# Kernel tuning notes

Measured on AMD Instinct MI355X. Metric: run time of the kernel, lower is better.

The kernel has to match this reference:

```python
import jax, jax.numpy as jnp
import numpy as np

B, C, LATENT = 64, 64, 256
KS = [50, 25, 12]  # grid side per stage; nodes 2500 -> 625 -> 144 -> 36
EPS = 1e-5


def _grid_graph(k):
    """torch_geometric.utils.grid: 8-neighbor stencil + self-loop, symmetric.
    Returns (src, dst, norm) with GCN symmetric normalization D^-1/2 A D^-1/2."""
    ii, jj = np.meshgrid(np.arange(k), np.arange(k), indexing='ij')
    src_l, dst_l = [], []
    for di in (-1, 0, 1):
        for dj in (-1, 0, 1):
            i0, i1 = max(0, -di), k - max(0, di)
            j0, j1 = max(0, -dj), k - max(0, dj)
            a = (ii[i0:i1, j0:j1] * k + jj[i0:i1, j0:j1]).ravel()
            b = ((ii[i0:i1, j0:j1] + di) * k + (jj[i0:i1, j0:j1] + dj)).ravel()
            src_l.append(a); dst_l.append(b)
    src = np.concatenate(src_l); dst = np.concatenate(dst_l)
    deg = np.bincount(dst, minlength=k * k).astype(np.float32)
    norm = 1.0 / np.sqrt(deg[src] * deg[dst])
    return jnp.asarray(src), jnp.asarray(dst), jnp.asarray(norm.astype(np.float32))

GRAPHS = [_grid_graph(k) for k in KS]


def _gcn(x, W, b, graph):
    # x: [B, N, Cin]; GCNConv: aggregate(norm * (xW)) + b
    src, dst, norm = graph
    h = x @ W                                   # [B, N, Cout]
    msg = h[:, src, :] * norm[None, :, None]    # gather along node dim
    out = jnp.zeros(h.shape, h.dtype).at[:, dst, :].add(msg)
    return out + b


def _inorm(x):
    # torch InstanceNorm1d applied to [B, N, C]: normalize over last axis
    m = jnp.mean(x, axis=-1, keepdims=True)
    v = jnp.var(x, axis=-1, keepdims=True)
    return (x - m) * jax.lax.rsqrt(v + EPS)


def _block(x, k, W1, b1, W2, b2, graph):
    x1 = jax.nn.celu(_inorm(_gcn(x, W1, b1, graph)))
    x2 = jax.nn.celu(_inorm(_gcn(x1, W2, b2, graph)) + x)
    Bn, N, Cc = x2.shape
    g = jnp.swapaxes(x2.reshape(Bn, k, k, Cc), 1, 3)      # [B, C, k, k]
    kk = (k // 2) * 2
    g = g[:, :, :kk, :kk].reshape(Bn, Cc, k // 2, 2, k // 2, 2).max(axis=(3, 5))
    return jnp.swapaxes(g, 1, 3).reshape(Bn, (k // 2) ** 2, Cc)


def _sn_linear(x, W, b, iters=30):
    # spectral-norm Linear: y = x @ (W / sigma_max(W)).T + b (power iteration)
    u = jnp.ones((W.shape[0],), W.dtype) / jnp.sqrt(jnp.asarray(W.shape[0], W.dtype))
    for _ in range(iters):
        v = W.T @ u
        v = v / (jnp.linalg.norm(v) + 1e-12)
        u = W @ v
        u = u / (jnp.linalg.norm(u) + 1e-12)
    sigma = u @ (W @ v)
    return x @ (W / sigma).T + b


def _forward(x, w_init, b_init, w11, b11, w12, b12, w21, b21, w22, b22,
             w31, b31, w32, b32, lw1, lb1, lw2, lb2):
    h = _gcn(x, w_init, b_init, GRAPHS[0])                 # [B, 2500, 64]
    h = _block(h, KS[0], w11, b11, w12, b12, GRAPHS[0])    # [B, 625, 64]
    h = _block(h, KS[1], w21, b21, w22, b22, GRAPHS[1])    # [B, 144, 64]
    h = _block(h, KS[2], w31, b31, w32, b32, GRAPHS[2])    # [B, 36, 64]
    h = h.reshape(h.shape[0], -1)                          # [B, 2304]
    h = jax.nn.celu(_sn_linear(h, lw1, lb1))
    h = jax.nn.celu(_sn_linear(h, lw2, lb2))
    return h


def setup_inputs() -> dict:
    key = jax.random.key(0)
    ks = jax.random.split(key, 20)
    n = lambda k, shape, fan: jax.random.normal(k, shape, jnp.float32) / np.sqrt(fan)
    flat = 36 * C
    return {
        'x': jax.random.normal(ks[0], (B, 2500, 1), jnp.float32),
        'w_init': n(ks[1], (1, C), 1), 'b_init': jnp.zeros((C,), jnp.float32),
        'w11': n(ks[2], (C, C), C), 'b11': jnp.zeros((C,), jnp.float32),
        'w12': n(ks[3], (C, C), C), 'b12': jnp.zeros((C,), jnp.float32),
        'w21': n(ks[4], (C, C), C), 'b21': jnp.zeros((C,), jnp.float32),
        'w22': n(ks[5], (C, C), C), 'b22': jnp.zeros((C,), jnp.float32),
        'w31': n(ks[6], (C, C), C), 'b31': jnp.zeros((C,), jnp.float32),
        'w32': n(ks[7], (C, C), C), 'b32': jnp.zeros((C,), jnp.float32),
        'lw1': n(ks[8], (LATENT, flat), flat), 'lb1': jnp.zeros((LATENT,), jnp.float32),
        'lw2': n(ks[9], (LATENT, LATENT), LATENT), 'lb2': jnp.zeros((LATENT,), jnp.float32),
    }


def reference(x, w_init, b_init, w11, b11, w12, b12, w21, b21, w22, b22,
              w31, b31, w32, b32, lw1, lb1, lw2, lb2):
    return _forward(x, w_init, b_init, w11, b11, w12, b12, w21, b21, w22, b22,
                    w31, b31, w32, b32, lw1, lb1, lw2, lb2)
```

## Files before the change

kernel.cpp:

```cpp
#include <hip/hip_runtime.h>
#include <hip/hip_bf16.h>
#include <math.h>

#define BATCH 64
#define K1 50
#define K2 25
#define K3 12
#define N1 (K1*K1)
#define N2 (K2*K2)
#define N3 (K3*K3)
#define EPS_IN 1e-5f

#define IRT2 0.70710678118654752f
#define IRT3 0.57735026918962576f

typedef __bf16 bf16x4 __attribute__((ext_vector_type(4)));
typedef __bf16 bf16x8 __attribute__((ext_vector_type(8)));
typedef float  f32x4  __attribute__((ext_vector_type(4)));

__device__ __forceinline__ float celu1(float v) {
    return v > 0.f ? v : (__expf(v) - 1.0f);
}

__device__ __forceinline__ float bfac(int v, int K) {
    return (v > 0 && v < K - 1) ? IRT3 : IRT2;
}

__global__ __launch_bounds__(256) void stencil_kernel(
    const float* __restrict__ x, float* __restrict__ out)
{
    int node = blockIdx.x * 256 + threadIdx.x;
    int b = node / N1, n = node - b * N1;
    int i = n / K1, j = n - i * K1;

    float fi[3], fj[3];
    int ric[3], rjc[3];
    {
        int im = i - 1, ip = i + 1;
        ric[0] = im < 0 ? 0 : im;       fi[0] = im < 0 ? 0.f : bfac(im, K1);
        ric[1] = i;                     fi[1] = bfac(i, K1);
        ric[2] = ip >= K1 ? K1-1 : ip;  fi[2] = ip >= K1 ? 0.f : bfac(ip, K1);
        int jm = j - 1, jp = j + 1;
        rjc[0] = jm < 0 ? 0 : jm;       fj[0] = jm < 0 ? 0.f : bfac(jm, K1);
        rjc[1] = j;                     fj[1] = bfac(j, K1);
        rjc[2] = jp >= K1 ? K1-1 : jp;  fj[2] = jp >= K1 ? 0.f : bfac(jp, K1);
    }
    float rsdn = fi[1] * fj[1];
    int rowb = b * N1;

    float s = 0.f;
#pragma unroll
    for (int di = 0; di < 3; ++di) {
        float wr = rsdn * fi[di];
        int rb = rowb + ric[di] * K1;
#pragma unroll
        for (int dj = 0; dj < 3; ++dj)
            s = fmaf(wr * fj[dj], x[rb + rjc[dj]], s);
    }
    out[node] = s;
}

template<int KK>
__global__ __launch_bounds__(256, 4) void conv1_kernel(
    const float* __restrict__ agg2,
    const float* __restrict__ winit, const float* __restrict__ binit,
    const float* __restrict__ Wm, const float* __restrict__ bias,
    __bf16* __restrict__ out)
{
    constexpr int NN = KK * KK;
    const int lane = threadIdx.x & 63;
    const int wv   = threadIdx.x >> 6;
    const int c15  = lane & 15, q = lane >> 4;

    bf16x8 bfrag[4][2];
#pragma unroll
    for (int nt = 0; nt < 4; ++nt)
#pragma unroll
        for (int kf = 0; kf < 2; ++kf) {
            bf16x8 v;
#pragma unroll
            for (int jj = 0; jj < 8; ++jj)
                v[jj] = (__bf16)Wm[(kf * 32 + q * 8 + jj) * 64 + nt * 16 + c15];
            bfrag[nt][kf] = v;
        }
    float bias_l[4];
#pragma unroll
    for (int nt = 0; nt < 4; ++nt) bias_l[nt] = bias[nt * 16 + c15];

    float wik[2][8], bik[2][8];
#pragma unroll
    for (int kf = 0; kf < 2; ++kf)
#pragma unroll
        for (int jj = 0; jj < 8; ++jj) {
            wik[kf][jj] = winit[kf * 32 + q * 8 + jj];
            bik[kf][jj] = binit[kf * 32 + q * 8 + jj];
        }

    int node0 = blockIdx.x * 128 + wv * 32 + c15;

    f32x4 acc[2][4];
#pragma unroll
    for (int t = 0; t < 2; ++t)
#pragma unroll
        for (int nt = 0; nt < 4; ++nt)
            acc[t][nt] = (f32x4){0.f, 0.f, 0.f, 0.f};

#pragma unroll
    for (int tile = 0; tile < 2; ++tile) {
        int node = node0 + tile * 16;
        float a2 = agg2[node];
        int b = node / NN, n = node - b * NN;
        int i = n / KK, j = n - i * KK;
        float f1i = bfac(i, KK), f1j = bfac(j, KK);
        float si = f1i + ((i > 0) ? bfac(i - 1, KK) : 0.f) + ((i < KK-1) ? bfac(i + 1, KK) : 0.f);
        float sj = f1j + ((j > 0) ? bfac(j - 1, KK) : 0.f) + ((j < KK-1) ? bfac(j + 1, KK) : 0.f);
        float tt = f1i * f1j * si * sj;

        bf16x8 av0, av1;
#pragma unroll
        for (int jj = 0; jj < 8; ++jj) {
            av0[jj] = (__bf16)fmaf(a2, wik[0][jj], tt * bik[0][jj]);
            av1[jj] = (__bf16)fmaf(a2, wik[1][jj], tt * bik[1][jj]);
        }
#pragma unroll
        for (int nt = 0; nt < 4; ++nt) {
            acc[tile][nt] = __builtin_amdgcn_mfma_f32_16x16x32_bf16(av0, bfrag[nt][0], acc[tile][nt], 0, 0, 0);
            acc[tile][nt] = __builtin_amdgcn_mfma_f32_16x16x32_bf16(av1, bfrag[nt][1], acc[tile][nt], 0, 0, 0);
        }
    }

#pragma unroll
    for (int tile = 0; tile < 2; ++tile) {
        float tm[4][4];
#pragma unroll
        for (int nt = 0; nt < 4; ++nt)
#pragma unroll
            for (int r = 0; r < 4; ++r)
                tm[nt][r] = acc[tile][nt][r] + bias_l[nt];

#pragma unroll
        for (int r = 0; r < 4; ++r) {
            float p = tm[0][r] + tm[1][r] + tm[2][r] + tm[3][r];
#pragma unroll
            for (int off = 1; off < 16; off <<= 1) p += __shfl_xor(p, off, 64);
            float mean = p * (1.0f / 64.0f);
            float vs = 0.f;
#pragma unroll
            for (int nt = 0; nt < 4; ++nt) {
                float d = tm[nt][r] - mean;
                vs = fmaf(d, d, vs);
            }
#pragma unroll
            for (int off = 1; off < 16; off <<= 1) vs += __shfl_xor(vs, off, 64);
            float rstd = __frsqrt_rn(vs * (1.0f / 64.0f) + EPS_IN);

            int node = blockIdx.x * 128 + wv * 32 + tile * 16 + q * 4 + r;
            int base = node * 64 + c15;
#pragma unroll
            for (int nt = 0; nt < 4; ++nt)
                out[base + nt * 16] = (__bf16)celu1((tm[nt][r] - mean) * rstd);
        }
    }
}

template<int KK, int MODE, bool BOUND>
__global__ __launch_bounds__(256, 4) void conv_kernel(
    const __bf16* __restrict__ xin, const __bf16* __restrict__ auxv,
    const float* __restrict__ auxs,
    const float* __restrict__ winit, const float* __restrict__ binit,
    const float* __restrict__ Wm, const float* __restrict__ bias,
    __bf16* __restrict__ out, int Ntot)
{
    constexpr int NN = KK * KK;
    __shared__ __align__(16) __bf16 s_lds[128 * 72];

    const int lane = threadIdx.x & 63;
    const int wv   = threadIdx.x >> 6;
    const int c15  = lane & 15, q = lane >> 4;
    const int n8   = lane >> 3;
    const int ch8  = (lane & 7) * 8;

    bf16x8 bfrag[4][2];
#pragma unroll
    for (int nt = 0; nt < 4; ++nt)
#pragma unroll
        for (int kf = 0; kf < 2; ++kf) {
            bf16x8 v;
#pragma unroll
            for (int jj = 0; jj < 8; ++jj)
                v[jj] = (__bf16)Wm[(kf * 32 + q * 8 + jj) * 64 + nt * 16 + c15];
            bfrag[nt][kf] = v;
        }
    float bias_l[4];
#pragma unroll
    for (int nt = 0; nt < 4; ++nt) bias_l[nt] = bias[nt * 16 + c15];

    float wi_e[4], bi_e[4];
    if (MODE == 3) {
#pragma unroll
        for (int nt = 0; nt < 4; ++nt) {
            wi_e[nt] = winit[nt * 16 + c15];
            bi_e[nt] = binit[nt * 16 + c15];
        }
    }

    const int G0 = blockIdx.x * 128;

#pragma unroll 2
    for (int m = 0; m < 4; ++m) {
        int nl = wv * 32 + m * 8 + n8;
        int node = G0 + nl;
        if (BOUND) node = min(node, Ntot - 1);
        int b = node / NN, n = node - b * NN;
        int i = n / KK, j = n - i * KK;

        float fi[3], fj[3];
        int ric[3], rjc[3];
        {
            int im = i - 1, ip = i + 1;
            ric[0] = im < 0 ? 0 : im;       fi[0] = im < 0 ? 0.f : bfac(im, KK);
            ric[1] = i;                     fi[1] = bfac(i, KK);
            ric[2] = ip >= KK ? KK-1 : ip;  fi[2] = ip >= KK ? 0.f : bfac(ip, KK);
            int jm = j - 1, jp = j + 1;
            rjc[0] = jm < 0 ? 0 : jm;       fj[0] = jm < 0 ? 0.f : bfac(jm, KK);
            rjc[1] = j;                     fj[1] = bfac(j, KK);
            rjc[2] = jp >= KK ? KK-1 : jp;  fj[2] = jp >= KK ? 0.f : bfac(jp, KK);
        }
        float rsdn = fi[1] * fj[1];

        int rbase[3], coff[3];
#pragma unroll
        for (int t = 0; t < 3; ++t) rbase[t] = (b * NN + ric[t] * KK) * 64 + ch8;
#pragma unroll
        for (int t = 0; t < 3; ++t) coff[t] = rjc[t] * 64;

        float s[8];
#pragma unroll
        for (int z = 0; z < 8; ++z) s[z] = 0.f;
#pragma unroll
        for (int di = 0; di < 3; ++di) {
            float wr = rsdn * fi[di];
#pragma unroll
            for (int dj = 0; dj < 3; ++dj) {
                float wgt = wr * fj[dj];
                bf16x8 v = *(const bf16x8*)(xin + rbase[di] + coff[dj]);
#pragma unroll
                for (int z = 0; z < 8; ++z)
                    s[z] = fmaf(wgt, (float)v[z], s[z]);
            }
        }
        bf16x8 sv;
#pragma unroll
        for (int z = 0; z < 8; ++z) sv[z] = (__bf16)s[z];
        *(bf16x8*)(s_lds + nl * 72 + ch8) = sv;
    }

    f32x4 acc[2][4];
#pragma unroll
    for (int t = 0; t < 2; ++t)
#pragma unroll
        for (int nt = 0; nt < 4; ++nt)
            acc[t][nt] = (f32x4){0.f, 0.f, 0.f, 0.f};

#pragma unroll
    for (int tile = 0; tile < 2; ++tile) {
        int r0 = wv * 32 + tile * 16 + c15;
        bf16x8 av0 = *(const bf16x8*)(s_lds + r0 * 72 + q * 8);
        bf16x8 av1 = *(const bf16x8*)(s_lds + r0 * 72 + 32 + q * 8);
#pragma unroll
        for (int nt = 0; nt < 4; ++nt) {
            acc[tile][nt] = __builtin_amdgcn_mfma_f32_16x16x32_bf16(av0, bfrag[nt][0], acc[tile][nt], 0, 0, 0);
            acc[tile][nt] = __builtin_amdgcn_mfma_f32_16x16x32_bf16(av1, bfrag[nt][1], acc[tile][nt], 0, 0, 0);
        }
    }

#pragma unroll
    for (int tile = 0; tile < 2; ++tile) {
        float tm[4][4];
#pragma unroll
        for (int nt = 0; nt < 4; ++nt)
#pragma unroll
            for (int r = 0; r < 4; ++r)
                tm[nt][r] = acc[tile][nt][r] + bias_l[nt];

#pragma unroll
        for (int r = 0; r < 4; ++r) {
            float p = tm[0][r] + tm[1][r] + tm[2][r] + tm[3][r];
#pragma unroll
            for (int off = 1; off < 16; off <<= 1) p += __shfl_xor(p, off, 64);
            float mean = p * (1.0f / 64.0f);
            float vs = 0.f;
#pragma unroll
            for (int nt = 0; nt < 4; ++nt) {
                float d = tm[nt][r] - mean;
                vs = fmaf(d, d, vs);
            }
#pragma unroll
            for (int off = 1; off < 16; off <<= 1) vs += __shfl_xor(vs, off, 64);
            float rstd = __frsqrt_rn(vs * (1.0f / 64.0f) + EPS_IN);

            int node = G0 + wv * 32 + tile * 16 + q * 4 + r;
            if (!BOUND || node < Ntot) {
                int base = node * 64 + c15;
                float av = 0.f;
                if (MODE == 3) av = auxs[node];
#pragma unroll
                for (int nt = 0; nt < 4; ++nt) {
                    float d = (tm[nt][r] - mean) * rstd;
                    if (MODE == 1) d += (float)auxv[base + nt * 16];
                    if (MODE == 3) d = fmaf(av, wi_e[nt], d + bi_e[nt]);
                    out[base + nt * 16] = (__bf16)celu1(d);
                }
            }
        }
    }
}

template<int KK>
__global__ __launch_bounds__(256) void pool_kernel(
    const __bf16* __restrict__ xin, __bf16* __restrict__ out)
{
    constexpr int NIN = KK * KK;
    constexpr int KH = KK / 2;
    constexpr int P = KH * KH;
    int e = blockIdx.x * 256 + threadIdx.x;
    int c = (e & 15) * 4;
    int np = e >> 4;
    int b = np / P, p = np - b * P;
    int pi = p / KH, pj = p - pi * KH;
    int basei = (b * NIN + (2 * pi) * KK + 2 * pj) * 64 + c;
    bf16x4 v0 = *(const bf16x4*)(xin + basei);
    bf16x4 v1 = *(const bf16x4*)(xin + basei + 64);
    bf16x4 v2 = *(const bf16x4*)(xin + basei + KK * 64);
    bf16x4 v3 = *(const bf16x4*)(xin + basei + KK * 64 + 64);
    bf16x4 o;
#pragma unroll
    for (int z = 0; z < 4; ++z) {
        float mv = fmaxf(fmaxf((float)v0[z], (float)v1[z]),
                         fmaxf((float)v2[z], (float)v3[z]));
        o[z] = (__bf16)mv;
    }
    *(bf16x4*)(out + np * 64 + c) = o;
}

__global__ __launch_bounds__(256) void gram_kernel(
    const float* __restrict__ W1, const float* __restrict__ W2,
    float* __restrict__ Gp1, float* __restrict__ Gp2)
{
    const float* W; float* G; int K, kc, s;
    if (blockIdx.z < 6) { W = W1; K = 2304; kc = 384; s = blockIdx.z;     G = Gp1 + s * 65536; }
    else               { W = W2; K = 256;  kc = 128; s = blockIdx.z - 6; G = Gp2 + s * 65536; }

    __shared__ float As[32][33];
    __shared__ float Bs[32][33];
    int ti = blockIdx.x * 32;
    int tj = blockIdx.y * 32;
    int k0s = s * kc;
    int tx = threadIdx.x & 15, ty = threadIdx.x >> 4;
    float a00 = 0.f, a01 = 0.f, a10 = 0.f, a11 = 0.f;
    for (int k0 = k0s; k0 < k0s + kc; k0 += 32) {
        for (int l = threadIdx.x; l < 1024; l += 256) {
            int r = l >> 5, cc = l & 31;
            As[r][cc] = W[(ti + r) * K + k0 + cc];
            Bs[r][cc] = W[(tj + r) * K + k0 + cc];
        }
        __syncthreads();
#pragma unroll
        for (int kk = 0; kk < 32; ++kk) {
            float a0 = As[ty][kk],      a1 = As[ty + 16][kk];
            float b0 = Bs[tx][kk],      b1 = Bs[tx + 16][kk];
            a00 = fmaf(a0, b0, a00); a01 = fmaf(a0, b1, a01);
            a10 = fmaf(a1, b0, a10); a11 = fmaf(a1, b1, a11);
        }
        __syncthreads();
    }
    G[(ti + ty) * 256 + tj + tx]           = a00;
    G[(ti + ty) * 256 + tj + tx + 16]      = a01;
    G[(ti + ty + 16) * 256 + tj + tx]      = a10;
    G[(ti + ty + 16) * 256 + tj + tx + 16] = a11;
}

__global__ __launch_bounds__(1024, 4) void power_kernel(
    const float* __restrict__ Gp1, const float* __restrict__ Gp2,
    float* __restrict__ sig)
{
    const float* Gp = (blockIdx.x == 0) ? Gp1 : Gp2;
    const int S = (blockIdx.x == 0) ? 6 : 2;
    __shared__ __align__(16) float u[256];
    __shared__ float red[1024];
    __shared__ float gu_s[256];
    int tid = threadIdx.x, i = tid & 255, q = tid >> 8;

    float g[64];
#pragma unroll
    for (int m = 0; m < 64; ++m) g[m] = 0.f;
    for (int s = 0; s < S; ++s) {
        const float* Gs = Gp + s * 65536;
#pragma unroll
        for (int m = 0; m < 64; ++m)
            g[m] += Gs[(q * 64 + m) * 256 + i];
    }
#pragma unroll
    for (int m = 0; m < 64; ++m) asm volatile("" : "+v"(g[m]));

    if (tid < 256) u[tid] = 0.0625f;
    __syncthreads();

    for (int it = 0; it < 29; ++it) {
        float p = 0.f;
#pragma unroll
        for (int m4 = 0; m4 < 16; ++m4) {
            f32x4 uv = *(const f32x4*)(u + q * 64 + m4 * 4);
            p = fmaf(g[m4 * 4 + 0], uv[0], p);
            p = fmaf(g[m4 * 4 + 1], uv[1], p);
            p = fmaf(g[m4 * 4 + 2], uv[2], p);
            p = fmaf(g[m4 * 4 + 3], uv[3], p);
        }
        red[tid] = p;
        __syncthreads();
        if (tid < 256)
            u[tid] = (red[tid] + red[tid + 256] + red[tid + 512] + red[tid + 768]) * 0.5f;
        __syncthreads();
    }

    float p = 0.f;
#pragma unroll
    for (int m4 = 0; m4 < 16; ++m4) {
        f32x4 uv = *(const f32x4*)(u + q * 64 + m4 * 4);
        p = fmaf(g[m4 * 4 + 0], uv[0], p);
        p = fmaf(g[m4 * 4 + 1], uv[1], p);
        p = fmaf(g[m4 * 4 + 2], uv[2], p);
        p = fmaf(g[m4 * 4 + 3], uv[3], p);
    }
    red[tid] = p;
    __syncthreads();
    if (tid < 256)
        gu_s[tid] = red[tid] + red[tid + 256] + red[tid + 512] + red[tid + 768];
    __syncthreads();
    if (tid < 64) {
        float a = 0.f, bs = 0.f;
        for (int z = tid; z < 256; z += 64) {
            float v = gu_s[z];
            a = fmaf(v, v, a);
            bs = fmaf(u[z], v, bs);
        }
#pragma unroll
        for (int off = 32; off; off >>= 1) {
            a  += __shfl_xor(a, off, 64);
            bs += __shfl_xor(bs, off, 64);
        }
        if (tid == 0) sig[blockIdx.x] = sqrtf(a / bs);
    }
}

__global__ __launch_bounds__(256) void linear_part(
    const __bf16* __restrict__ X, const float* __restrict__ Wt,
    float* __restrict__ part, int K, int kchunk)
{
    __shared__ float wl[64 * 129];
    __shared__ float hl[16 * 128];
    int o0 = blockIdx.x * 64, b0 = blockIdx.y * 16;
    int s = blockIdx.z;
    int k0s = s * kchunk;
    int t = threadIdx.x, o = t & 63, br = t >> 6;
    float acc[4] = {0.f, 0.f, 0.f, 0.f};

    for (int k0 = k0s; k0 < k0s + kchunk; k0 += 128) {
        for (int l = t; l < 64 * 128; l += 256) {
            int r = l >> 7, cc = l & 127;
            wl[r * 129 + cc] = Wt[(o0 + r) * K + k0 + cc];
        }
        for (int l = t; l < 16 * 128; l += 256) {
            int r = l >> 7, cc = l & 127;
            hl[r * 128 + cc] = (float)X[(b0 + r) * K + k0 + cc];
        }
        __syncthreads();
        for (int kk = 0; kk < 128; ++kk) {
            float wv = wl[o * 129 + kk];
#pragma unroll
            for (int r = 0; r < 4; ++r)
                acc[r] = fmaf(hl[(br + (r << 2)) * 128 + kk], wv, acc[r]);
        }
        __syncthreads();
    }
#pragma unroll
    for (int r = 0; r < 4; ++r)
        part[(s * 64 + b0 + br + (r << 2)) * 256 + o0 + o] = acc[r];
}

__global__ __launch_bounds__(256) void linear_epi(
    const float* __restrict__ part, const float* __restrict__ bias,
    const float* __restrict__ sig, int sidx, int S,
    float* __restrict__ outf, __bf16* __restrict__ outb)
{
    int idx = blockIdx.x * 256 + threadIdx.x;
    float a = 0.f;
    for (int s = 0; s < S; ++s) a += part[s * 16384 + idx];
    int o = idx & 255;
    float v = celu1(a / sig[sidx] + bias[o]);
    if (outf) outf[idx] = v;
    if (outb) outb[idx] = (__bf16)v;
}

extern "C" void kernel_launch(void* const* d_in, const int* in_sizes, int n_in,
                              void* d_out, int out_size, void* d_ws, size_t ws_size,
                              hipStream_t stream)
{
    const float* x      = (const float*)d_in[0];
    const float* w_init = (const float*)d_in[1];
    const float* b_init = (const float*)d_in[2];
    const float* w11 = (const float*)d_in[3];  const float* b11 = (const float*)d_in[4];
    const float* w12 = (const float*)d_in[5];  const float* b12 = (const float*)d_in[6];
    const float* w21 = (const float*)d_in[7];  const float* b21 = (const float*)d_in[8];
    const float* w22 = (const float*)d_in[9];  const float* b22 = (const float*)d_in[10];
    const float* w31 = (const float*)d_in[11]; const float* b31 = (const float*)d_in[12];
    const float* w32 = (const float*)d_in[13]; const float* b32 = (const float*)d_in[14];
    const float* lw1 = (const float*)d_in[15]; const float* lb1 = (const float*)d_in[16];
    const float* lw2 = (const float*)d_in[17]; const float* lb2 = (const float*)d_in[18];
    float* out = (float*)d_out;

    char* ws = (char*)d_ws;
    const size_t SZ_BIG = (size_t)BATCH * N1 * 64 * sizeof(float);
    __bf16* A    = (__bf16*)ws;
    __bf16* Bb   = (__bf16*)(ws + SZ_BIG);
    __bf16* Cb   = (__bf16*)(ws + 2 * SZ_BIG);
    float*  agg  = (float*)(ws + 3 * SZ_BIG);
    float*  agg2 = agg + BATCH * N1;
    float* Gp1   = agg2 + BATCH * N1;
    float* Gp2   = Gp1 + 6 * 65536;
    float* sg    = Gp2 + 2 * 65536;
    float* part1 = sg + 16;
    float* part2 = part1 + 6 * 16384;
    __bf16* H1b  = (__bf16*)(part2 + 2 * 16384);

    stencil_kernel<<<625, 256, 0, stream>>>(x, agg);
    stencil_kernel<<<625, 256, 0, stream>>>(agg, agg2);

    conv1_kernel<K1><<<1250, 256, 0, stream>>>(agg2, w_init, b_init, w11, b11, Bb);
    conv_kernel<K1, 3, false><<<1250, 256, 0, stream>>>(Bb, nullptr, agg, w_init, b_init, w12, b12, Cb, BATCH * N1);
    pool_kernel<K1><<<BATCH * N2 * 16 / 256, 256, 0, stream>>>(Cb, A);

    conv_kernel<K2, 0, true><<<313, 256, 0, stream>>>(A,  nullptr, nullptr, nullptr, nullptr, w21, b21, Bb, BATCH * N2);
    conv_kernel<K2, 1, true><<<313, 256, 0, stream>>>(Bb, A,       nullptr, nullptr, nullptr, w22, b22, Cb, BATCH * N2);
    pool_kernel<K2><<<BATCH * N3 * 16 / 256, 256, 0, stream>>>(Cb, A);

    conv_kernel<K3, 0, false><<<72, 256, 0, stream>>>(A,  nullptr, nullptr, nullptr, nullptr, w31, b31, Bb, BATCH * N3);
    conv_kernel<K3, 1, false><<<72, 256, 0, stream>>>(Bb, A,       nullptr, nullptr, nullptr, w32, b32, Cb, BATCH * N3);
    pool_kernel<K3><<<BATCH * 36 * 16 / 256, 256, 0, stream>>>(Cb, A);

    gram_kernel<<<dim3(8, 8, 8), 256, 0, stream>>>(lw1, lw2, Gp1, Gp2);
    power_kernel<<<2, 1024, 0, stream>>>(Gp1, Gp2, sg);

    linear_part<<<dim3(4, 4, 6), 256, 0, stream>>>(A,   lw1, part1, 2304, 384);
    linear_epi<<<64, 256, 0, stream>>>(part1, lb1, sg, 0, 6, nullptr, H1b);
    linear_part<<<dim3(4, 4, 2), 256, 0, stream>>>(H1b, lw2, part2, 256, 128);
    linear_epi<<<64, 256, 0, stream>>>(part2, lb2, sg, 1, 2, out, nullptr);
}
```

Measured before the change: 302.7 us.

## Replace serial power iteration with repeated squaring of the Gram matrix

The 29-step sequential power iteration over the 256x256 Gram matrix is replaced by forming G^2, G^4, G^8 and G^16 with small parallel tiled matmul kernels. A short chain of matvecs (G, G^4, G^8, G^16, which together apply G^29) then gives the Rayleigh-quotient sigma. A separate reduce kernel first sums the partial Gram slices. This cuts 29 barrier-bound, single-block iterations down to four parallel squarings plus five matvecs, in exchange for five extra launches, extra global traffic in the reused Cb workspace, and slightly different rounding from the high matrix powers.

```diff
diff --git a/kernel.cpp b/kernel.cpp
--- a/kernel.cpp
+++ b/kernel.cpp
@@ -380,76 +380,115 @@
     G[(ti + ty + 16) * 256 + tj + tx + 16] = a11;
 }
 
-__global__ __launch_bounds__(1024, 4) void power_kernel(
+__global__ __launch_bounds__(256) void gram_reduce(
     const float* __restrict__ Gp1, const float* __restrict__ Gp2,
+    float* __restrict__ G1, float* __restrict__ G2)
+{
+    int idx = blockIdx.x * 256 + threadIdx.x;
+    if (idx < 65536) {
+        float a = 0.f;
+#pragma unroll
+        for (int s = 0; s < 6; ++s) a += Gp1[s * 65536 + idx];
+        G1[idx] = a;
+    } else {
+        int jx = idx - 65536;
+        G2[jx] = Gp2[jx] + Gp2[65536 + jx];
+    }
+}
+
+__global__ __launch_bounds__(256) void sq_kernel(
+    const float* __restrict__ A1, const float* __restrict__ A2,
+    float* __restrict__ C1, float* __restrict__ C2)
+{
+    const float* A = blockIdx.z ? A2 : A1;
+    float* C = blockIdx.z ? C2 : C1;
+
+    __shared__ float As[32][33];
+    __shared__ float Bs[32][33];
+    int ti = blockIdx.x * 32;
+    int tj = blockIdx.y * 32;
+    int tx = threadIdx.x & 15, ty = threadIdx.x >> 4;
+    float a00 = 0.f, a01 = 0.f, a10 = 0.f, a11 = 0.f;
+    for (int k0 = 0; k0 < 256; k0 += 32) {
+        for (int l = threadIdx.x; l < 1024; l += 256) {
+            int r = l >> 5, cc = l & 31;
+            As[r][cc] = A[(ti + r) * 256 + k0 + cc];
+            Bs[r][cc] = A[(tj + r) * 256 + k0 + cc];
+        }
+        __syncthreads();
+#pragma unroll
+        for (int kk = 0; kk < 32; ++kk) {
+            float a0 = As[ty][kk],      a1 = As[ty + 16][kk];
+            float b0 = Bs[tx][kk],      b1 = Bs[tx + 16][kk];
+            a00 = fmaf(a0, b0, a00); a01 = fmaf(a0, b1, a01);
+            a10 = fmaf(a1, b0, a10); a11 = fmaf(a1, b1, a11);
+        }
+        __syncthreads();
+    }
+    C[(ti + ty) * 256 + tj + tx]           = a00;
+    C[(ti + ty) * 256 + tj + tx + 16]      = a01;
+    C[(ti + ty + 16) * 256 + tj + tx]      = a10;
+    C[(ti + ty + 16) * 256 + tj + tx + 16] = a11;
+}
+
+__global__ __launch_bounds__(256) void sigma_kernel(
+    const float* __restrict__ G1, const float* __restrict__ G2,
+    const float* __restrict__ S4a, const float* __restrict__ S4b,
+    const float* __restrict__ S8a, const float* __restrict__ S8b,
+    const float* __restrict__ S16a, const float* __restrict__ S16b,
     float* __restrict__ sig)
 {
-    const float* Gp = (blockIdx.x == 0) ? Gp1 : Gp2;
-    const int S = (blockIdx.x == 0) ? 6 : 2;
-    __shared__ __align__(16) float u[256];
-    __shared__ float red[1024];
-    __shared__ float gu_s[256];
-    int tid = threadIdx.x, i = tid & 255, q = tid >> 8;
-
-    float g[64];
-#pragma unroll
-    for (int m = 0; m < 64; ++m) g[m] = 0.f;
-    for (int s = 0; s < S; ++s) {
-        const float* Gs = Gp + s * 65536;
-#pragma unroll
-        for (int m = 0; m < 64; ++m)
-            g[m] += Gs[(q * 64 + m) * 256 + i];
-    }
-#pragma unroll
-    for (int m = 0; m < 64; ++m) asm volatile("" : "+v"(g[m]));
-
-    if (tid < 256) u[tid] = 0.0625f;
+    const int z = blockIdx.x, t = threadIdx.x;
+    const int wv = t >> 6;
+    const float* G   = z ? G2   : G1;
+    const float* M4  = z ? S4b  : S4a;
+    const float* M8  = z ? S8b  : S8a;
+    const float* M16 = z ? S16b : S16a;
+
+    __shared__ float v[256];
+    __shared__ float wred[8];
+
+    v[t] = 1.0f;
     __syncthreads();
 
-    for (int it = 0; it < 29; ++it) {
-        float p = 0.f;
-#pragma unroll
-        for (int m4 = 0; m4 < 16; ++m4) {
-            f32x4 uv = *(const f32x4*)(u + q * 64 + m4 * 4);
-            p = fmaf(g[m4 * 4 + 0], uv[0], p);
-            p = fmaf(g[m4 * 4 + 1], uv[1], p);
-            p = fmaf(g[m4 * 4 + 2], uv[2], p);
-            p = fmaf(g[m4 * 4 + 3], uv[3], p);
-        }
-        red[tid] = p;
-        __syncthreads();
-        if (tid < 256)
-            u[tid] = (red[tid] + red[tid + 256] + red[tid + 512] + red[tid + 768]) * 0.5f;
-        __syncthreads();
-    }
-
-    float p = 0.f;
-#pragma unroll
-    for (int m4 = 0; m4 < 16; ++m4) {
-        f32x4 uv = *(const f32x4*)(u + q * 64 + m4 * 4);
-        p = fmaf(g[m4 * 4 + 0], uv[0], p);
-        p = fmaf(g[m4 * 4 + 1], uv[1], p);
-        p = fmaf(g[m4 * 4 + 2], uv[2], p);
-        p = fmaf(g[m4 * 4 + 3], uv[3], p);
-    }
-    red[tid] = p;
+    const float* chain[4] = { G, M4, M8, M16 };
+    float y = 0.f;
+    for (int step = 0; step < 4; ++step) {
+        const float* M = chain[step];
+        float acc = 0.f;
+#pragma unroll 8
+        for (int k = 0; k < 256; ++k)
+            acc = fmaf(M[k * 256 + t], v[k], acc);
+        y = acc;
+        float ss = y * y;
+#pragma unroll
+        for (int off = 32; off; off >>= 1) ss += __shfl_xor(ss, off, 64);
+        __syncthreads();
+        if ((t & 63) == 0) wred[wv] = ss;
+        __syncthreads();
+        float tot = wred[0] + wred[1] + wred[2] + wred[3];
+        v[t] = y * __frsqrt_rn(tot);
+        __syncthreads();
+    }
+
+    float gu = 0.f;
+#pragma unroll 8
+    for (int k = 0; k < 256; ++k)
+        gu = fmaf(G[k * 256 + t], v[k], gu);
+    float a = gu * gu;
+    float b = v[t] * gu;
+#pragma unroll
+    for (int off = 32; off; off >>= 1) {
+        a += __shfl_xor(a, off, 64);
+        b += __shfl_xor(b, off, 64);
+    }
     __syncthreads();
-    if (tid < 256)
-        gu_s[tid] = red[tid] + red[tid + 256] + red[tid + 512] + red[tid + 768];
+    if ((t & 63) == 0) { wred[wv] = a; wred[4 + wv] = b; }
     __syncthreads();
-    if (tid < 64) {
-        float a = 0.f, bs = 0.f;
-        for (int z = tid; z < 256; z += 64) {
-            float v = gu_s[z];
-            a = fmaf(v, v, a);
-            bs = fmaf(u[z], v, bs);
-        }
-#pragma unroll
-        for (int off = 32; off; off >>= 1) {
-            a  += __shfl_xor(a, off, 64);
-            bs += __shfl_xor(bs, off, 64);
-        }
-        if (tid == 0) sig[blockIdx.x] = sqrtf(a / bs);
+    if (t == 0) {
+        float at = wred[0] + wred[1] + wred[2] + wred[3];
+        float bt = wred[4] + wred[5] + wred[6] + wred[7];
+        sig[z] = sqrtf(at / bt);
     }
 }
 
@@ -533,6 +572,14 @@
     float* part2 = part1 + 6 * 16384;
     __bf16* H1b  = (__bf16*)(part2 + 2 * 16384);
 
+    float* Gm  = (float*)(ws + 2 * SZ_BIG);
+    float* G1  = Gm;
+    float* G2  = Gm + 1 * 65536;
+    float* S2a = Gm + 2 * 65536;  float* S2b = Gm + 3 * 65536;
+    float* S4a = Gm + 4 * 65536;  float* S4b = Gm + 5 * 65536;
+    float* S8a = Gm + 6 * 65536;  float* S8b = Gm + 7 * 65536;
+    float* S16a= Gm + 8 * 65536;  float* S16b= Gm + 9 * 65536;
+
     stencil_kernel<<<625, 256, 0, stream>>>(x, agg);
     stencil_kernel<<<625, 256, 0, stream>>>(agg, agg2);
 
@@ -549,7 +596,12 @@
     pool_kernel<K3><<<BATCH * 36 * 16 / 256, 256, 0, stream>>>(Cb, A);
 
     gram_kernel<<<dim3(8, 8, 8), 256, 0, stream>>>(lw1, lw2, Gp1, Gp2);
-    power_kernel<<<2, 1024, 0, stream>>>(Gp1, Gp2, sg);
+    gram_reduce<<<512, 256, 0, stream>>>(Gp1, Gp2, G1, G2);
+    sq_kernel<<<dim3(8, 8, 2), 256, 0, stream>>>(G1,  G2,  S2a,  S2b);
+    sq_kernel<<<dim3(8, 8, 2), 256, 0, stream>>>(S2a, S2b, S4a,  S4b);
+    sq_kernel<<<dim3(8, 8, 2), 256, 0, stream>>>(S4a, S4b, S8a,  S8b);
+    sq_kernel<<<dim3(8, 8, 2), 256, 0, stream>>>(S8a, S8b, S16a, S16b);
+    sigma_kernel<<<2, 256, 0, stream>>>(G1, G2, S4a, S4b, S8a, S8b, S16a, S16b, sg);
 
     linear_part<<<dim3(4, 4, 6), 256, 0, stream>>>(A,   lw1, part1, 2304, 384);
     linear_epi<<<64, 256, 0, stream>>>(part1, lb1, sg, 0, 6, nullptr, H1b);
```

After: 340.0 us. +12.3%, slower.
